# Performance work log

Measured on AMD Instinct MI355X. Metric: run time of the kernel, lower is better.

The kernel has to match this reference:

```python
import jax, jax.numpy as jnp
import numpy as np

B, S, D = 2, 2048, 512
H = 8
G = 4
LAMBDA_INIT = 0.2  # 0.8 - 0.6*exp(-0.3*(layer_idx-1)) with layer_idx=1
EPS = 1e-5


def setup_inputs() -> dict:
    key = jax.random.key(0)
    ks = jax.random.split(key, 16)
    n = jax.random.normal
    return {
        "x": n(ks[0], (B, S, D), jnp.float32),
        "K1_w": n(ks[1], (D, D), jnp.float32) * 0.02,
        "K1_b": n(ks[2], (D,), jnp.float32) * 0.02,
        "Q1_w": n(ks[3], (D, D), jnp.float32) * 0.02,
        "K2_w": n(ks[4], (D, D), jnp.float32) * 0.02,
        "K2_b": n(ks[5], (D,), jnp.float32) * 0.02,
        "Q2_w": n(ks[6], (D, D), jnp.float32) * 0.02,
        "V_w": n(ks[7], (D, D), jnp.float32) * 0.02,
        "lambda_q1": n(ks[8], (H, 1), jnp.float32),
        "lambda_k1": n(ks[9], (H, 1), jnp.float32),
        "lambda_q2": n(ks[10], (H, 1), jnp.float32),
        "lambda_k2": n(ks[11], (H, 1), jnp.float32),
        "gn_w": jnp.ones((D,), jnp.float32),
        "gn_b": jnp.zeros((D,), jnp.float32),
        "out_w": n(ks[12], (D, D), jnp.float32) * 0.02,
        "out_b": n(ks[13], (D,), jnp.float32) * 0.02,
    }


def reference(x, K1_w, K1_b, Q1_w, K2_w, K2_b, Q2_w, V_w,
              lambda_q1, lambda_k1, lambda_q2, lambda_k2,
              gn_w, gn_b, out_w, out_b):
    b, s, d = x.shape
    hd = d // H

    def heads(t):  # (b,s,d) -> (b,H,s,hd)
        return t.reshape(b, s, H, hd).transpose(0, 2, 1, 3)

    q1 = heads(x @ Q1_w.T)
    k1 = heads(x @ K1_w.T + K1_b)
    q2 = heads(x @ Q2_w.T)
    k2 = heads(x @ K2_w.T + K2_b)
    v = heads(x @ V_w.T)

    scale = hd ** 0.5
    a1 = jax.nn.softmax(jnp.einsum('bhqd,bhkd->bhqk', q1, k1) / scale, axis=-1)
    a2 = jax.nn.softmax(jnp.einsum('bhqd,bhkd->bhqk', q2, k2) / scale, axis=-1)

    lam = (jnp.exp(lambda_q1 * lambda_k1)
           - jnp.exp(lambda_q2 * lambda_k2) + LAMBDA_INIT)  # (H,1)
    attn = a1 - lam.reshape(1, H, 1, 1) * a2

    o = jnp.einsum('bhqk,bhkd->bhqd', attn, v)
    o = o.transpose(0, 2, 1, 3).reshape(b, s, d)

    # GroupNorm over channels: input (b, d, s), groups G normalize over (d/G, s)
    xc = o.transpose(0, 2, 1).reshape(b, G, d // G, s)
    mu = xc.mean(axis=(2, 3), keepdims=True)
    var = xc.var(axis=(2, 3), keepdims=True)
    xn = ((xc - mu) * jax.lax.rsqrt(var + EPS)).reshape(b, d, s)
    xn = xn * gn_w[None, :, None] + gn_b[None, :, None]

    y = xn.transpose(0, 2, 1) @ out_w.T + out_b
    return y
```

## Files before the change

kernel.cpp:

```cpp
#include <hip/hip_runtime.h>
#include <hip/hip_bf16.h>

typedef __bf16 bf16;
typedef __attribute__((ext_vector_type(4))) __bf16 bf16x4;
typedef __attribute__((ext_vector_type(8))) __bf16 bf16x8;
typedef __attribute__((ext_vector_type(4))) float f32x4;

#define MFMA16(a, b, c) __builtin_amdgcn_mfma_f32_16x16x32_bf16((a), (b), (c), 0, 0, 0)

static constexpr float EPS = 1e-5f;
static constexpr float LAMBDA_INIT = 0.2f;
static constexpr float LOG2E = 1.44269504088896340736f;

__device__ __forceinline__ bf16x8 cvt8(const float* p) {
    const f32x4 a = *(const f32x4*)p;
    const f32x4 b = *(const f32x4*)(p + 4);
    bf16x8 r;
    r[0] = (bf16)a[0]; r[1] = (bf16)a[1]; r[2] = (bf16)a[2]; r[3] = (bf16)a[3];
    r[4] = (bf16)b[0]; r[5] = (bf16)b[1]; r[6] = (bf16)b[2]; r[7] = (bf16)b[3];
    return r;
}

__device__ __forceinline__ void gload_lds16(const void* g, void* l) {
    __builtin_amdgcn_global_load_lds(
        (const __attribute__((address_space(1))) unsigned int*)g,
        (__attribute__((address_space(3))) unsigned int*)l,
        16, 0, 0);
}

__global__ __launch_bounds__(256) void prep_kernel(
    const float* __restrict__ x,
    const float* __restrict__ q1w, const float* __restrict__ k1w,
    const float* __restrict__ q2w, const float* __restrict__ k2w,
    const float* __restrict__ vw,
    const float* __restrict__ ow, const float* __restrict__ gnw,
    const float* __restrict__ gnb,
    bf16* __restrict__ xb, bf16* __restrict__ wb,
    bf16* __restrict__ owg, float* __restrict__ S0, float* __restrict__ stats)
{
    const int tid = threadIdx.x;
    if (blockIdx.x < 1664) {
        const size_t base = ((size_t)blockIdx.x * 256 + tid) * 8;
        if (base < 2097152) {
            *(bf16x8*)(xb + base) = cvt8(x + base);
        } else {
            const size_t wbase = base - 2097152;
            const int wsel = (int)(wbase >> 18);
            const size_t off = wbase & 262143;
            const float* W = (wsel == 0) ? q1w : (wsel == 1) ? k1w :
                             (wsel == 2) ? q2w : (wsel == 3) ? k2w : vw;
            *(bf16x8*)(wb + wbase) = cvt8(W + off);
        }
        return;
    }

    const int pb = blockIdx.x - 1664;
    if (pb == 0 && tid < 16) stats[tid] = 0.f;

    const int wave = tid >> 6, lane = tid & 63;
    const int c0 = lane * 8;
    const f32x4 gw0 = *(const f32x4*)(gnw + c0);
    const f32x4 gw1 = *(const f32x4*)(gnw + c0 + 4);
    const f32x4 gb0 = *(const f32x4*)(gnb + c0);
    const f32x4 gb1 = *(const f32x4*)(gnb + c0 + 4);

#pragma unroll
    for (int rr = 0; rr < 4; ++rr) {
        const int n = pb * 16 + wave * 4 + rr;
        const float* p = ow + (size_t)n * 512 + c0;
        const f32x4 w0 = *(const f32x4*)p;
        const f32x4 w1 = *(const f32x4*)(p + 4);
        bf16x8 og;
        float s = 0.f;
#pragma unroll
        for (int j = 0; j < 4; ++j) {
            og[j]     = (bf16)(w0[j] * gw0[j]);
            og[4 + j] = (bf16)(w1[j] * gw1[j]);
            s += gb0[j] * w0[j] + gb1[j] * w1[j];
        }
        *(bf16x8*)(owg + (size_t)n * 512 + c0) = og;
#pragma unroll
        for (int off = 1; off < 64; off <<= 1) s += __shfl_xor(s, off, 64);
        if (lane == 0) S0[n] = s;
    }
}

__global__ __launch_bounds__(256) void proj_kernel(
    const bf16* __restrict__ xb, const bf16* __restrict__ wb,
    const float* __restrict__ k1b, const float* __restrict__ k2b,
    bf16* __restrict__ q1o, bf16* __restrict__ k1o,
    bf16* __restrict__ q2o, bf16* __restrict__ k2o,
    bf16* __restrict__ vto)
{
    __shared__ __align__(16) bf16 sh[32768];
    bf16* const As0 = sh;
    bf16* const As1 = sh + 8192;
    bf16* const Bs0 = sh + 16384;
    bf16* const Bs1 = sh + 24576;

    const int tid = threadIdx.x;
    const int wave = tid >> 6, lane = tid & 63;
    const int l15 = lane & 15, quad = lane >> 4;
    const int wm = wave >> 1, wn = wave & 1;

    const int swzb = (blockIdx.x & 7) * 80 + (blockIdx.x >> 3);
    const int mb = swzb / 20;
    const int nb = swzb % 20;
    const int wsel = nb >> 2;
    const int nrow0 = (nb & 3) * 128;

    const int srow = lane >> 3;
    const int scol = 8 * ((lane & 7) ^ srow);
    const bf16* ag = xb + (size_t)(mb * 128 + srow) * 512 + scol;
    const bf16* bg = wb + (size_t)(wsel * 512 + nrow0 + srow) * 512 + scol;

    f32x4 acc[4][4];
#pragma unroll
    for (int i = 0; i < 4; ++i)
#pragma unroll
        for (int j = 0; j < 4; ++j)
            acc[i][j] = (f32x4){0.f, 0.f, 0.f, 0.f};

#define STAGE_PROJ(abuf, bbuf, s) do {                                         \
    const int k0_ = (s) * 64;                                                  \
    _Pragma("unroll")                                                          \
    for (int c_ = 0; c_ < 4; ++c_) {                                           \
        const int chunk_ = wave * 4 + c_;                                      \
        gload_lds16(ag + (size_t)(chunk_ * 8) * 512 + k0_, (abuf) + chunk_ * 512); \
        gload_lds16(bg + (size_t)(chunk_ * 8) * 512 + k0_, (bbuf) + chunk_ * 512); \
    }                                                                          \
} while (0)

    STAGE_PROJ(As0, Bs0, 0);
    __syncthreads();

    const int ka = 8 * (quad ^ (l15 & 7));

    for (int s = 0; s < 8; ++s) {
        const bf16* Ac = (s & 1) ? As1 : As0;
        const bf16* Bc = (s & 1) ? Bs1 : Bs0;
        if (s < 7) {
            if (s & 1) STAGE_PROJ(As0, Bs0, s + 1);
            else       STAGE_PROJ(As1, Bs1, s + 1);
        }

        bf16x8 al[4], ah[4], bl[4], bh_[4];
#pragma unroll
        for (int i = 0; i < 4; ++i) {
            const bf16* p = Ac + (wm * 64 + i * 16 + l15) * 64;
            al[i] = *(const bf16x8*)(p + ka);
            ah[i] = *(const bf16x8*)(p + (ka ^ 32));
        }
#pragma unroll
        for (int j = 0; j < 4; ++j) {
            const bf16* p = Bc + (wn * 64 + j * 16 + l15) * 64;
            bl[j]  = *(const bf16x8*)(p + ka);
            bh_[j] = *(const bf16x8*)(p + (ka ^ 32));
        }

#pragma unroll
        for (int i = 0; i < 4; ++i)
#pragma unroll
            for (int j = 0; j < 4; ++j) {
                acc[i][j] = MFMA16(al[i], bl[j], acc[i][j]);
                acc[i][j] = MFMA16(ah[i], bh_[j], acc[i][j]);
            }

        __syncthreads();
    }

    const int bidx = mb >> 4;
    const int sbase = (mb & 15) * 128;
    const float scale = (wsel == 0 || wsel == 2) ? 0.125f * LOG2E : 1.0f;

    if (wsel != 4) {
        bf16* const T = sh;
        const int swzq = quad << 4;
#pragma unroll
        for (int j = 0; j < 4; ++j) {
            const int nl = wn * 64 + j * 16 + l15;
            const int ncol = nrow0 + nl;
            float bias = 0.f;
            if (wsel == 1) bias = k1b[ncol];
            if (wsel == 3) bias = k2b[ncol];
            const int nswz = nl ^ swzq;
#pragma unroll
            for (int i = 0; i < 4; ++i) {
                const int mbase = wm * 64 + i * 16 + quad * 4;
#pragma unroll
                for (int r = 0; r < 4; ++r)
                    T[(mbase + r) * 128 + nswz] = (bf16)(acc[i][j][r] * scale + bias);
            }
        }
        __syncthreads();

        bf16* const dst = (wsel == 0) ? q1o : (wsel == 1) ? k1o :
                          (wsel == 2) ? q2o : k2o;
#pragma unroll
        for (int hsel = 0; hsel < 2; ++hsel) {
            const int h = (nrow0 >> 6) + hsel;
            bf16* db = dst + ((size_t)(bidx * 8 + h) * 2048 + sbase) * 64;
#pragma unroll
            for (int ps = 0; ps < 4; ++ps) {
                const int idx = (ps * 256 + tid) * 8;
                const int m = idx >> 6, hd = idx & 63;
                const bf16x8 v = *(const bf16x8*)(
                    T + m * 128 + ((hsel * 64 + hd) ^ (((m >> 2) & 3) << 4)));
                *(bf16x8*)(db + idx) = v;
            }
        }
    } else {
        bf16* const Tt = sh;
#pragma unroll
        for (int j = 0; j < 4; ++j) {
            const int nl = wn * 64 + j * 16 + l15;
            const int hd = (nrow0 + nl) & 63;
            const int xh = (hd >> 1) & 3;
            const int swz = (nl & 7) << 2;
#pragma unroll
            for (int i = 0; i < 4; ++i) {
                const int colb = (wm * 64 + (i >> 1) * 32 + ((quad ^ xh) << 3)
                                  + ((i & 1) << 2)) ^ swz;
                bf16x4 pk;
#pragma unroll
                for (int r = 0; r < 4; ++r) pk[r] = (bf16)acc[i][j][r];
                *(bf16x4*)(Tt + nl * 132 + colb) = pk;
            }
        }
        __syncthreads();

#pragma unroll
        for (int ps = 0; ps < 8; ++ps) {
            const int rown = ps * 16 + (tid >> 4);
            const int seg = tid & 15;
            const int swz = (rown & 7) << 2;
            const bf16x4 lo = *(const bf16x4*)(Tt + rown * 132 + ((seg * 8) ^ swz));
            const bf16x4 hi = *(const bf16x4*)(Tt + rown * 132 + ((seg * 8 + 4) ^ swz));
            const int ncol = nrow0 + rown;
            const int h = ncol >> 6, hd = ncol & 63;
            bf16x8 v;
            v[0] = lo[0]; v[1] = lo[1]; v[2] = lo[2]; v[3] = lo[3];
            v[4] = hi[0]; v[5] = hi[1]; v[6] = hi[2]; v[7] = hi[3];
            *(bf16x8*)(vto + ((size_t)(bidx * 8 + h) * 64 + hd) * 2048
                       + sbase + seg * 8) = v;
        }
    }
#undef STAGE_PROJ
}

__global__ __launch_bounds__(512, 4) void attn_kernel(
    const bf16* __restrict__ q1, const bf16* __restrict__ k1,
    const bf16* __restrict__ q2, const bf16* __restrict__ k2,
    const bf16* __restrict__ vt,
    const float* __restrict__ lq1, const float* __restrict__ lk1,
    const float* __restrict__ lq2, const float* __restrict__ lk2,
    bf16* __restrict__ o, float* __restrict__ stats)
{
    __shared__ __align__(16) bf16 smem[2][12288];
    __shared__ float lbuf[8][2][16];
    __shared__ float sred[2][2];

    const int tid = threadIdx.x;
    const int wave = tid >> 6;
    const int lane = tid & 63;
    const int l15 = lane & 15, quad = lane >> 4;
    const int kg = wave >> 2;
    const int w4 = wave & 3;
    const int qp = w4 & 1;
    const int st = w4 >> 1;

    const int rid = (blockIdx.x & 7) * 64 + (blockIdx.x >> 3);
    const int bh = rid >> 5;
    const int qt = rid & 31;
    const int b = bh >> 3, h = bh & 7;

    const bf16* k1t = k1 + (size_t)bh * 2048 * 64;
    const bf16* k2t = k2 + (size_t)bh * 2048 * 64;
    const bf16* vtt = vt + (size_t)bh * 64 * 2048;

    const bf16* qs = st ? q2 : q1;
    const int qrowA = qt * 64 + qp * 32 + l15;
    const bf16* qpA = qs + ((size_t)bh * 2048 + qrowA) * 64 + quad * 8;
    const bf16x8 qA0 = *(const bf16x8*)(qpA);
    const bf16x8 qA1 = *(const bf16x8*)(qpA + 32);
    const bf16x8 qB0 = *(const bf16x8*)(qpA + 16 * 64);
    const bf16x8 qB1 = *(const bf16x8*)(qpA + 16 * 64 + 32);

    const int sw = wave & 3;
    const int skey0 = (wave < 4) ? 0 : 1024;
    const size_t ksrc0 = (size_t)(skey0 + sw * 8 + (lane >> 3)) * 64
                       + 8 * ((lane & 7) ^ (lane >> 3));
    const size_t vsrc0 = (size_t)(sw * 16 + (lane >> 2)) * 2048 + skey0 + (lane & 3) * 8;

#define STAGE_ATTN(buf, itv) do {                                   \
    const size_t koff_ = ksrc0 + (size_t)(itv) * 32 * 64;           \
    gload_lds16(k1t + koff_, (buf) + wave * 512);                   \
    gload_lds16(k2t + koff_, (buf) + 4096 + wave * 512);            \
    gload_lds16(vtt + vsrc0 + (itv) * 32, (buf) + 8192 + wave * 512); \
} while (0)

    const int koffa = 8 * (quad ^ (l15 & 7));
    const int koffb = 8 * ((quad + 4) ^ (l15 & 7));
    const int vsw = 8 * (quad ^ ((l15 >> 1) & 3));

    f32x4 OA[4], OB[4];
    float lA = 0.f, lB = 0.f;
#pragma unroll
    for (int t = 0; t < 4; ++t) {
        OA[t] = (f32x4){0.f, 0.f, 0.f, 0.f};
        OB[t] = (f32x4){0.f, 0.f, 0.f, 0.f};
    }

    STAGE_ATTN(smem[0], 0);
    __syncthreads();

    for (int it = 0; it < 32; ++it) {
        const bf16* sb = smem[it & 1];
        if (it < 31) STAGE_ATTN(smem[(it & 1) ^ 1], it + 1);

        const bf16* kr = sb + st * 4096 + kg * 2048;
        const bf16* vr = sb + 8192 + kg * 2048;

        const bf16x8 kt0a = *(const bf16x8*)(kr + l15 * 64 + koffa);
        const bf16x8 kt0b = *(const bf16x8*)(kr + l15 * 64 + koffb);
        const bf16x8 kt1a = *(const bf16x8*)(kr + (16 + l15) * 64 + koffa);
        const bf16x8 kt1b = *(const bf16x8*)(kr + (16 + l15) * 64 + koffb);
        const bf16x8 v0 = *(const bf16x8*)(vr + l15 * 32 + vsw);
        const bf16x8 v1 = *(const bf16x8*)(vr + (16 + l15) * 32 + vsw);
        const bf16x8 v2 = *(const bf16x8*)(vr + (32 + l15) * 32 + vsw);
        const bf16x8 v3 = *(const bf16x8*)(vr + (48 + l15) * 32 + vsw);

        const f32x4 z = (f32x4){0.f, 0.f, 0.f, 0.f};
        __builtin_amdgcn_s_setprio(1);
        f32x4 sA0 = MFMA16(kt0a, qA0, z);  sA0 = MFMA16(kt0b, qA1, sA0);
        f32x4 sA1 = MFMA16(kt1a, qA0, z);  sA1 = MFMA16(kt1b, qA1, sA1);
        f32x4 sB0 = MFMA16(kt0a, qB0, z);  sB0 = MFMA16(kt0b, qB1, sB0);
        f32x4 sB1 = MFMA16(kt1a, qB0, z);  sB1 = MFMA16(kt1b, qB1, sB1);
        __builtin_amdgcn_s_setprio(0);

        bf16x8 bA, bB;
#pragma unroll
        for (int r = 0; r < 4; ++r) {
            float e;
            e = __builtin_amdgcn_exp2f(sA0[r]); lA += e; bA[r]     = (bf16)e;
            e = __builtin_amdgcn_exp2f(sA1[r]); lA += e; bA[4 + r] = (bf16)e;
            e = __builtin_amdgcn_exp2f(sB0[r]); lB += e; bB[r]     = (bf16)e;
            e = __builtin_amdgcn_exp2f(sB1[r]); lB += e; bB[4 + r] = (bf16)e;
        }

        __builtin_amdgcn_s_setprio(1);
        OA[0] = MFMA16(v0, bA, OA[0]);
        OA[1] = MFMA16(v1, bA, OA[1]);
        OA[2] = MFMA16(v2, bA, OA[2]);
        OA[3] = MFMA16(v3, bA, OA[3]);
        OB[0] = MFMA16(v0, bB, OB[0]);
        OB[1] = MFMA16(v1, bB, OB[1]);
        OB[2] = MFMA16(v2, bB, OB[2]);
        OB[3] = MFMA16(v3, bB, OB[3]);
        __builtin_amdgcn_s_setprio(0);

        __syncthreads();
    }

    lA += __shfl_xor(lA, 16, 64);  lA += __shfl_xor(lA, 32, 64);
    lB += __shfl_xor(lB, 16, 64);  lB += __shfl_xor(lB, 32, 64);
    if (lane < 16) {
        lbuf[wave][0][lane] = lA;
        lbuf[wave][1][lane] = lB;
    }
    __syncthreads();

    f32x4* rb = (f32x4*)smem;
    if (kg == 1) {
        f32x4* dst = rb + w4 * 512;
#pragma unroll
        for (int t = 0; t < 4; ++t) {
            dst[t * 64 + lane]       = OA[t];
            dst[(4 + t) * 64 + lane] = OB[t];
        }
    }
    __syncthreads();
    if (kg == 0) {
        const f32x4* src = rb + w4 * 512;
#pragma unroll
        for (int t = 0; t < 4; ++t) {
            OA[t] += src[t * 64 + lane];
            OB[t] += src[(4 + t) * 64 + lane];
        }
    }
    __syncthreads();

    if (kg == 0 && st == 1) {
        f32x4* dst = rb + qp * 512;
#pragma unroll
        for (int t = 0; t < 4; ++t) {
            dst[t * 64 + lane]       = OA[t];
            dst[(4 + t) * 64 + lane] = OB[t];
        }
    }
    __syncthreads();

    float ssum = 0.f, ssq = 0.f;
    if (kg == 0 && st == 0) {
        const f32x4* src = rb + qp * 512;
        const float L1A = lA + lbuf[4 + qp][0][l15];
        const float L1B = lB + lbuf[4 + qp][1][l15];
        const float L2A = lbuf[2 + qp][0][l15] + lbuf[6 + qp][0][l15];
        const float L2B = lbuf[2 + qp][1][l15] + lbuf[6 + qp][1][l15];
        const float lam = __expf(lq1[h] * lk1[h]) - __expf(lq2[h] * lk2[h]) + LAMBDA_INIT;
        const float i1A = 1.f / L1A, i2A = lam / L2A;
        const float i1B = 1.f / L1B, i2B = lam / L2B;
        const size_t rowA = (size_t)(b * 2048 + qt * 64 + qp * 32 + l15) * 512 + h * 64;
        const size_t rowB = rowA + 16 * 512;
#pragma unroll
        for (int t = 0; t < 4; ++t) {
            const f32x4 o2A = src[t * 64 + lane];
            const f32x4 o2B = src[(4 + t) * 64 + lane];
#pragma unroll
            for (int r = 0; r < 4; ++r) {
                const float vA = OA[t][r] * i1A - o2A[r] * i2A;
                const float vB = OB[t][r] * i1B - o2B[r] * i2B;
                ssum += vA + vB;
                ssq += vA * vA + vB * vB;
                o[rowA + t * 16 + quad * 4 + r] = (bf16)vA;
                o[rowB + t * 16 + quad * 4 + r] = (bf16)vB;
            }
        }
    }
#pragma unroll
    for (int off = 1; off < 64; off <<= 1) {
        ssum += __shfl_xor(ssum, off, 64);
        ssq += __shfl_xor(ssq, off, 64);
    }
    if (kg == 0 && st == 0 && lane == 0) { sred[qp][0] = ssum; sred[qp][1] = ssq; }
    __syncthreads();
    if (tid == 0) {
        const float s0 = sred[0][0] + sred[1][0];
        const float s1 = sred[0][1] + sred[1][1];
        const int bg = b * 4 + (h >> 1);
        atomicAdd(&stats[bg * 2], s0);
        atomicAdd(&stats[bg * 2 + 1], s1);
    }
#undef STAGE_ATTN
}

__global__ __launch_bounds__(256) void out_gemm_kernel(
    const bf16* __restrict__ o, const bf16* __restrict__ owg,
    const float* __restrict__ S0, const float* __restrict__ stats,
    const float* __restrict__ ob, float* __restrict__ y)
{
    __shared__ __align__(16) bf16 sh[24576];

    const int tid = threadIdx.x;
    const int wave = tid >> 6, lane = tid & 63;
    const int l15 = lane & 15, quad = lane >> 4;

    const int swzb = (blockIdx.x & 7) * 64 + (blockIdx.x >> 3);
    const int mb = swzb >> 3;
    const int nb = swzb & 7;
    const int b = mb >> 5;

    const float N = 128.f * 2048.f;
    float mu[4], rs[4];
#pragma unroll
    for (int g = 0; g < 4; ++g) {
        const float m = stats[(b * 4 + g) * 2] / N;
        const float var = stats[(b * 4 + g) * 2 + 1] / N - m * m;
        mu[g] = m;
        rs[g] = rsqrtf(var + EPS);
    }

    const int srow = lane >> 3;
    const int scol = 8 * ((lane & 7) ^ srow);
    const bf16* ag = o + (size_t)(mb * 64 + srow) * 512 + scol;
    const bf16* bg = owg + (size_t)(nb * 64 + srow) * 512 + scol;

#define STAGE_OUT(abuf, bbuf, s) do {                                          \
    const int k0_ = (s) * 64;                                                  \
    _Pragma("unroll")                                                          \
    for (int c_ = 0; c_ < 2; ++c_) {                                           \
        const int chunk_ = wave * 2 + c_;                                      \
        gload_lds16(ag + (size_t)(chunk_ * 8) * 512 + k0_, (abuf) + chunk_ * 512); \
        gload_lds16(bg + (size_t)(chunk_ * 8) * 512 + k0_, (bbuf) + chunk_ * 512); \
    }                                                                          \
} while (0)

    f32x4 acc[4], tot[4];
#pragma unroll
    for (int i = 0; i < 4; ++i) {
        acc[i] = (f32x4){0.f, 0.f, 0.f, 0.f};
        tot[i] = (f32x4){0.f, 0.f, 0.f, 0.f};
    }
    float s1g[4];
    float s1p = 0.f;
#pragma unroll
    for (int g = 0; g < 4; ++g) s1g[g] = 0.f;

    STAGE_OUT(sh, sh + 12288, 0);
    STAGE_OUT(sh + 4096, sh + 12288 + 4096, 1);

    const int ka = 8 * (quad ^ (l15 & 7));

    int cur = 0;
    for (int kk = 0; kk < 8; ++kk) {
        if (kk < 7) {
            asm volatile("s_waitcnt vmcnt(4) lgkmcnt(0)\ns_barrier" ::: "memory");
        } else {
            asm volatile("s_waitcnt vmcnt(0) lgkmcnt(0)\ns_barrier" ::: "memory");
        }
        __builtin_amdgcn_sched_barrier(0);

        const bf16* Ac = sh + cur * 4096;
        const bf16* Bc = sh + 12288 + cur * 4096;
        const int n2 = (cur == 0) ? 2 : cur - 1;
        if (kk < 6) STAGE_OUT(sh + n2 * 4096, sh + 12288 + n2 * 4096, kk + 2);

        bf16x8 al[4], ah[4];
#pragma unroll
        for (int i = 0; i < 4; ++i) {
            const bf16* p = Ac + (i * 16 + l15) * 64;
            al[i] = *(const bf16x8*)(p + ka);
            ah[i] = *(const bf16x8*)(p + (ka ^ 32));
        }
        const bf16* pb = Bc + (wave * 16 + l15) * 64;
        const bf16x8 bl = *(const bf16x8*)(pb + ka);
        const bf16x8 bh = *(const bf16x8*)(pb + (ka ^ 32));

#pragma unroll
        for (int i = 0; i < 4; ++i) {
            acc[i] = MFMA16(al[i], bl, acc[i]);
            acc[i] = MFMA16(ah[i], bh, acc[i]);
        }

#pragma unroll
        for (int j = 0; j < 8; ++j) s1p += (float)bl[j] + (float)bh[j];

        if (kk & 1) {
            const int g = kk >> 1;
#pragma unroll
            for (int i = 0; i < 4; ++i) {
#pragma unroll
                for (int r = 0; r < 4; ++r) tot[i][r] += rs[g] * acc[i][r];
                acc[i] = (f32x4){0.f, 0.f, 0.f, 0.f};
            }
            float sg = s1p + __shfl_xor(s1p, 16, 64);
            sg += __shfl_xor(sg, 32, 64);
            s1g[g] = sg;
            s1p = 0.f;
        }

        cur = (cur == 2) ? 0 : cur + 1;
    }
    __syncthreads();

    const int ncol = nb * 64 + wave * 16 + l15;
    float bias = S0[ncol] + ob[ncol];
#pragma unroll
    for (int g = 0; g < 4; ++g) bias -= mu[g] * rs[g] * s1g[g];

    float* const Tf = (float*)sh;
    const int nl = wave * 16 + l15;
#pragma unroll
    for (int i = 0; i < 4; ++i) {
        const int mbase = i * 16 + quad * 4;
#pragma unroll
        for (int r = 0; r < 4; ++r)
            Tf[(mbase + r) * 64 + (nl ^ (quad << 4))] = tot[i][r] + bias;
    }
    __syncthreads();

#pragma unroll
    for (int ps = 0; ps < 4; ++ps) {
        const int idx = (ps * 256 + tid) * 4;
        const int m = idx >> 6, n4 = idx & 63;
        const f32x4 v = *(const f32x4*)(Tf + m * 64 + (n4 ^ (((m >> 2) & 3) << 4)));
        *(f32x4*)(y + (size_t)(mb * 64 + m) * 512 + nb * 64 + n4) = v;
    }
#undef STAGE_OUT
}

extern "C" void kernel_launch(void* const* d_in, const int* in_sizes, int n_in,
                              void* d_out, int out_size, void* d_ws, size_t ws_size,
                              hipStream_t stream)
{
    const float* x   = (const float*)d_in[0];
    const float* K1w = (const float*)d_in[1];
    const float* K1b = (const float*)d_in[2];
    const float* Q1w = (const float*)d_in[3];
    const float* K2w = (const float*)d_in[4];
    const float* K2b = (const float*)d_in[5];
    const float* Q2w = (const float*)d_in[6];
    const float* Vw  = (const float*)d_in[7];
    const float* lq1 = (const float*)d_in[8];
    const float* lk1 = (const float*)d_in[9];
    const float* lq2 = (const float*)d_in[10];
    const float* lk2 = (const float*)d_in[11];
    const float* gnw = (const float*)d_in[12];
    const float* gnb = (const float*)d_in[13];
    const float* Ow  = (const float*)d_in[14];
    const float* Ob  = (const float*)d_in[15];

    const size_t SZ = (size_t)2 * 8 * 2048 * 64;
    bf16* q1 = (bf16*)d_ws;
    bf16* k1 = q1 + SZ;
    bf16* q2 = k1 + SZ;
    bf16* k2 = q2 + SZ;
    bf16* vt = k2 + SZ;
    bf16* o  = vt + SZ;
    bf16* xb = o;
    bf16* wb = o + SZ;
    bf16* owg = wb + (size_t)2560 * 512;
    float* S0 = (float*)(owg + 512 * 512);
    float* stats = S0 + 512;

    prep_kernel<<<1696, 256, 0, stream>>>(x, Q1w, K1w, Q2w, K2w, Vw,
                                          Ow, gnw, gnb, xb, wb, owg, S0, stats);
    proj_kernel<<<640, 256, 0, stream>>>(xb, wb, K1b, K2b,
                                         q1, k1, q2, k2, vt);
    attn_kernel<<<512, 512, 0, stream>>>(q1, k1, q2, k2, vt,
                                         lq1, lk1, lq2, lk2, o, stats);
    out_gemm_kernel<<<512, 256, 0, stream>>>(o, owg, S0, stats, Ob,
                                             (float*)d_out);
}
```

Measured before the change: 168.6 us.

## Software-pipeline attention loop: overlap PV MFMAs with next tile's exp

Restructures the attention main loop so the P·V matrix multiplies for iteration i-1 are issued after the QK multiplies of iteration i, which interleaves MFMA work with the exp2 softmax work. A third LDS buffer keeps the previous tile's V alive while the next tile is staged, and an epilogue finishes the last PV step. This raises LDS use per block from two to three 24 KB buffers, which may reduce occupancy at the declared four blocks per CU.

```diff
diff --git a/kernel.cpp b/kernel.cpp
--- a/kernel.cpp
+++ b/kernel.cpp
@@ -256,7 +256,7 @@
     const float* __restrict__ lq2, const float* __restrict__ lk2,
     bf16* __restrict__ o, float* __restrict__ stats)
 {
-    __shared__ __align__(16) bf16 smem[2][12288];
+    __shared__ __align__(16) bf16 smem[3][12288];
     __shared__ float lbuf[8][2][16];
     __shared__ float sred[2][2];
 
@@ -311,24 +311,22 @@
         OB[t] = (f32x4){0.f, 0.f, 0.f, 0.f};
     }
 
+    bf16x8 pbA, pbB;
+
     STAGE_ATTN(smem[0], 0);
     __syncthreads();
 
+    int cur = 0;
     for (int it = 0; it < 32; ++it) {
-        const bf16* sb = smem[it & 1];
-        if (it < 31) STAGE_ATTN(smem[(it & 1) ^ 1], it + 1);
-
-        const bf16* kr = sb + st * 4096 + kg * 2048;
-        const bf16* vr = sb + 8192 + kg * 2048;
-
+        const int nxt = (cur == 2) ? 0 : cur + 1;
+        const int prv = (cur == 0) ? 2 : cur - 1;
+        if (it < 31) STAGE_ATTN(smem[nxt], it + 1);
+
+        const bf16* kr = smem[cur] + st * 4096 + kg * 2048;
         const bf16x8 kt0a = *(const bf16x8*)(kr + l15 * 64 + koffa);
         const bf16x8 kt0b = *(const bf16x8*)(kr + l15 * 64 + koffb);
         const bf16x8 kt1a = *(const bf16x8*)(kr + (16 + l15) * 64 + koffa);
         const bf16x8 kt1b = *(const bf16x8*)(kr + (16 + l15) * 64 + koffb);
-        const bf16x8 v0 = *(const bf16x8*)(vr + l15 * 32 + vsw);
-        const bf16x8 v1 = *(const bf16x8*)(vr + (16 + l15) * 32 + vsw);
-        const bf16x8 v2 = *(const bf16x8*)(vr + (32 + l15) * 32 + vsw);
-        const bf16x8 v3 = *(const bf16x8*)(vr + (48 + l15) * 32 + vsw);
 
         const f32x4 z = (f32x4){0.f, 0.f, 0.f, 0.f};
         __builtin_amdgcn_s_setprio(1);
@@ -338,6 +336,24 @@
         f32x4 sB1 = MFMA16(kt1a, qB0, z);  sB1 = MFMA16(kt1b, qB1, sB1);
         __builtin_amdgcn_s_setprio(0);
 
+        if (it > 0) {
+            const bf16* vp = smem[prv] + 8192 + kg * 2048;
+            const bf16x8 v0 = *(const bf16x8*)(vp + l15 * 32 + vsw);
+            const bf16x8 v1 = *(const bf16x8*)(vp + (16 + l15) * 32 + vsw);
+            const bf16x8 v2 = *(const bf16x8*)(vp + (32 + l15) * 32 + vsw);
+            const bf16x8 v3 = *(const bf16x8*)(vp + (48 + l15) * 32 + vsw);
+            __builtin_amdgcn_s_setprio(1);
+            OA[0] = MFMA16(v0, pbA, OA[0]);
+            OA[1] = MFMA16(v1, pbA, OA[1]);
+            OA[2] = MFMA16(v2, pbA, OA[2]);
+            OA[3] = MFMA16(v3, pbA, OA[3]);
+            OB[0] = MFMA16(v0, pbB, OB[0]);
+            OB[1] = MFMA16(v1, pbB, OB[1]);
+            OB[2] = MFMA16(v2, pbB, OB[2]);
+            OB[3] = MFMA16(v3, pbB, OB[3]);
+            __builtin_amdgcn_s_setprio(0);
+        }
+
         bf16x8 bA, bB;
 #pragma unroll
         for (int r = 0; r < 4; ++r) {
@@ -347,19 +363,27 @@
             e = __builtin_amdgcn_exp2f(sB0[r]); lB += e; bB[r]     = (bf16)e;
             e = __builtin_amdgcn_exp2f(sB1[r]); lB += e; bB[4 + r] = (bf16)e;
         }
-
-        __builtin_amdgcn_s_setprio(1);
-        OA[0] = MFMA16(v0, bA, OA[0]);
-        OA[1] = MFMA16(v1, bA, OA[1]);
-        OA[2] = MFMA16(v2, bA, OA[2]);
-        OA[3] = MFMA16(v3, bA, OA[3]);
-        OB[0] = MFMA16(v0, bB, OB[0]);
-        OB[1] = MFMA16(v1, bB, OB[1]);
-        OB[2] = MFMA16(v2, bB, OB[2]);
-        OB[3] = MFMA16(v3, bB, OB[3]);
-        __builtin_amdgcn_s_setprio(0);
+        pbA = bA;  pbB = bB;
 
         __syncthreads();
+        cur = nxt;
+    }
+
+    {
+        const int prv = (cur == 0) ? 2 : cur - 1;
+        const bf16* vp = smem[prv] + 8192 + kg * 2048;
+        const bf16x8 v0 = *(const bf16x8*)(vp + l15 * 32 + vsw);
+        const bf16x8 v1 = *(const bf16x8*)(vp + (16 + l15) * 32 + vsw);
+        const bf16x8 v2 = *(const bf16x8*)(vp + (32 + l15) * 32 + vsw);
+        const bf16x8 v3 = *(const bf16x8*)(vp + (48 + l15) * 32 + vsw);
+        OA[0] = MFMA16(v0, pbA, OA[0]);
+        OA[1] = MFMA16(v1, pbA, OA[1]);
+        OA[2] = MFMA16(v2, pbA, OA[2]);
+        OA[3] = MFMA16(v3, pbA, OA[3]);
+        OB[0] = MFMA16(v0, pbB, OB[0]);
+        OB[1] = MFMA16(v1, pbB, OB[1]);
+        OB[2] = MFMA16(v2, pbB, OB[2]);
+        OB[3] = MFMA16(v3, pbB, OB[3]);
     }
 
     lA += __shfl_xor(lA, 16, 64);  lA += __shfl_xor(lA, 32, 64);
```

Result: no change. 169.5 us (+0.5%).
